# Kernel tuning notes

Measured on AMD Instinct MI355X. Metric: run time of the kernel, lower is better.

## Reference

```python
import jax, jax.numpy as jnp
import numpy as np

DIGITS = 4
SAMPLES = 2048
BATCH = 512
ALPHA = 0.1


def setup_inputs() -> dict:
    key = jax.random.key(0)
    k1, k2, k3 = jax.random.split(key, 3)
    n1_logits = jax.random.normal(k1, (BATCH, DIGITS, 10), dtype=jnp.float32)
    # sample counters start at ones and stay positive; keep them in (1, 2)
    counters = jax.random.uniform(k2, (DIGITS, 10), dtype=jnp.float32) + 1.0
    s = jax.random.randint(k3, (BATCH,), 0, 10 ** DIGITS, dtype=jnp.int32)
    return {"n1_logits": n1_logits, "counters": counters, "s": s}


def reference(n1_logits, counters, s):
    B, D, _ = n1_logits.shape
    S = SAMPLES
    key = jax.random.key(42)
    digit_idx = jnp.arange(10, dtype=jnp.int32)
    constraint = jnp.zeros((B, S), dtype=jnp.int32)
    samples_list = []
    for i in range(D):
        if i == 0:
            maxim = (s // 10 ** (D - 1)).astype(jnp.int32)
            minim = jnp.maximum(0, maxim - 9)
        else:
            maxim = ((s // 10 ** (D - 1 - i)) % 10).astype(jnp.int32)
            minim = jnp.zeros_like(maxim)
        # [B, S, 10]: per-digit logits repeated over samples, counter penalty
        probs = n1_logits[:, i, None, :] - ALPHA * jnp.log(counters[i])[None, None, :]
        probs = jnp.broadcast_to(probs, (B, S, 10))
        # restrict to [minim, maxim] per batch row (equiv of per-row tf.concat with -inf pads)
        valid = (digit_idx[None, :] >= minim[:, None]) & (digit_idx[None, :] <= maxim[:, None])  # [B,10]
        probs_cut = jnp.where(valid[:, None, :], probs, -jnp.inf)
        logits = jnp.where(constraint[..., None] == 1, probs, probs_cut)
        key, sub = jax.random.split(key)
        samp = jax.random.categorical(sub, logits).astype(jnp.int32)  # [B,S]
        constraint = jnp.maximum(jnp.where(samp == maxim[:, None], 0, 1), constraint)
        samples_list.append(samp)
    n1_samples = jnp.stack(samples_list, axis=-1)  # [B,S,D]
    multiplier = (10 ** jnp.arange(D - 1, -1, -1)).astype(jnp.int32)  # [D]
    n1_summed = jnp.sum(n1_samples * multiplier, axis=-1)  # [B,S]
    n2 = s[:, None] - n1_summed  # [B,S], guaranteed in [0, 10^D)
    # sample_weights: per-row multiplicity of each sampled value (unique_with_counts+gather)
    V = 10 ** D
    row = jnp.arange(B, dtype=jnp.int32)[:, None]
    hist = jnp.zeros((B, V), jnp.float32).at[row, n1_summed].add(1.0)
    weights = jnp.take_along_axis(hist, n1_summed, axis=1)  # [B,S]
    # decimalise n2 via cumulative-quotient + sorted shift trick (faithful to tf code)
    mult2 = jnp.concatenate(
        [jnp.full((D - 1,), 10, dtype=jnp.int32), jnp.zeros((1,), dtype=jnp.int32)]
    )  # [10,...,10,0]
    n2d = n2[..., None] // multiplier  # [B,S,D] cumulative quotients
    n2d = n2d - jnp.sort(n2d * mult2, axis=-1)
    return n1_samples[..., None], n2d[..., None], weights
```

## Files before the change

kernel.cpp:

```cpp
#include <hip/hip_runtime.h>
#include <stdint.h>
#include <stddef.h>


namespace {

constexpr int B = 512, S = 2048, D = 4, NC = 10;
constexpr int BS = B * S;
constexpr size_t OUT1_OFF = (size_t)BS * D;
constexpr size_t OUT2_OFF = (size_t)BS * D * 2;

constexpr uint32_t crotl(uint32_t x, int d) { return (x << d) | (x >> (32 - d)); }
struct CU2 { uint32_t a, b; };
constexpr CU2 ctf(uint32_t k0, uint32_t k1, uint32_t c0, uint32_t c1) {
  uint32_t ks2 = k0 ^ k1 ^ 0x1BD11BDAu;
  uint32_t x0 = c0 + k0, x1 = c1 + k1;
  const int rots[8] = {13, 15, 26, 6, 17, 29, 16, 24};
  const uint32_t ks[3] = {k0, k1, ks2};
  for (int blk = 0; blk < 5; ++blk) {
    for (int j = 0; j < 4; ++j) {
      int r = rots[(blk & 1) * 4 + j];
      x0 += x1; x1 = crotl(x1, r); x1 ^= x0;
    }
    x0 += ks[(blk + 1) % 3];
    x1 += ks[(blk + 2) % 3] + (uint32_t)(blk + 1);
  }
  return CU2{x0, x1};
}

struct Keys { uint32_t kx[D]; uint32_t ky[D]; };
constexpr Keys make_keys() {
  Keys K{};
  uint32_t a = 0u, b = 42u;
  for (int i = 0; i < D; ++i) {
    CU2 sub = ctf(a, b, 0u, 1u);
    CU2 nk  = ctf(a, b, 0u, 0u);
    K.kx[i] = sub.a; K.ky[i] = sub.b;
    a = nk.a; b = nk.b;
  }
  return K;
}
constexpr Keys KEYS = make_keys();

struct U2 { uint32_t a, b; };
__device__ __forceinline__ uint32_t rotl32(uint32_t x, int d) {
  return (x << d) | (x >> (32 - d));
}
__device__ __forceinline__ U2 tf(uint32_t k0, uint32_t k1, uint32_t c0, uint32_t c1) {
  uint32_t ks2 = k0 ^ k1 ^ 0x1BD11BDAu;
  uint32_t x0 = c0 + k0, x1 = c1 + k1;
#define TF_RND(r) { x0 += x1; x1 = rotl32(x1, (r)); x1 ^= x0; }
  TF_RND(13) TF_RND(15) TF_RND(26) TF_RND(6)   x0 += k1;  x1 += ks2 + 1u;
  TF_RND(17) TF_RND(29) TF_RND(16) TF_RND(24)  x0 += ks2; x1 += k0 + 2u;
  TF_RND(13) TF_RND(15) TF_RND(26) TF_RND(6)   x0 += k0;  x1 += k1 + 3u;
  TF_RND(17) TF_RND(29) TF_RND(16) TF_RND(24)  x0 += k1;  x1 += ks2 + 4u;
  TF_RND(13) TF_RND(15) TF_RND(26) TF_RND(6)   x0 += ks2; x1 += k0 + 5u;
#undef TF_RND
  return U2{x0, x1};
}

__device__ __forceinline__ float xla_logf(float a) {
  uint32_t bits = __float_as_uint(a);
  float e = (float)((int)(bits >> 23) - 126);
  float m = __uint_as_float((bits & 0x007fffffu) | 0x3f000000u);
  bool mlt = m < 0.707106781186547524f;
  float tmp = mlt ? m : 0.0f;
  float x = __fsub_rn(m, 1.0f);
  e = __fsub_rn(e, mlt ? 1.0f : 0.0f);
  x = __fadd_rn(x, tmp);
  float x2 = __fmul_rn(x, x);
  float x3 = __fmul_rn(x2, x);
  float y  = __fmaf_rn(7.0376836292e-2f,  x, -1.1514610310e-1f);
  float y1 = __fmaf_rn(-1.2420140846e-1f, x,  1.4249322787e-1f);
  float y2 = __fmaf_rn(2.0000714765e-1f,  x, -2.4999993993e-1f);
  y  = __fmaf_rn(y,  x,  1.1676998740e-1f);
  y1 = __fmaf_rn(y1, x, -1.6668057665e-1f);
  y2 = __fmaf_rn(y2, x,  3.3333331174e-1f);
  y  = __fmaf_rn(y, x3, y1);
  y  = __fmaf_rn(y, x3, y2);
  y  = __fmul_rn(y, x3);
  y1 = __fmul_rn(e, -2.12194440e-4f);
  tmp = __fmul_rn(x2, 0.5f);
  y = __fadd_rn(y, y1);
  x = __fsub_rn(x, tmp);
  y2 = __fmul_rn(e, 0.693359375f);
  x = __fadd_rn(x, y);
  x = __fadd_rn(x, y2);
  return x;
}

__device__ __forceinline__ float gumbel_from_bits(uint32_t bits) {
  float f = __fsub_rn(__uint_as_float((bits >> 9) | 0x3f800000u), 1.0f);
  float u = __fadd_rn(f, 1.17549435e-38f);
  float l1 = xla_logf(u);
  float l2 = xla_logf(-l1);
  return -l2;
}

__global__ __launch_bounds__(1024) void fused_kernel(
    const float* __restrict__ logits,
    const float* __restrict__ counters,
    const int*   __restrict__ s_in,
    float* __restrict__ out)
{
  __shared__ int hist[10000];
  __shared__ float s_p[D * NC];
  const int t = threadIdx.x;
  const int b = blockIdx.x;

  for (int i = t; i < 10000; i += 1024) hist[i] = 0;
  if (t < D * NC) {
    s_p[t] = __fsub_rn(logits[b * D * NC + t],
                       __fmul_rn(0.1f, xla_logf(counters[t])));
  }
  __syncthreads();

  const int sval = s_in[b];
  const int mx[D] = {sval / 1000, (sval / 100) % 10, (sval / 10) % 10, sval % 10};

  int vals[2];
#pragma unroll
  for (int k = 0; k < 2; ++k) {
    const int sidx = t + k * 1024;
    const uint32_t n0 = (uint32_t)(b * S + sidx) * (uint32_t)NC;
    int con = 0;
    int dg[D];
#pragma unroll
    for (int i = 0; i < D; ++i) {
      const uint32_t kx = KEYS.kx[i], ky = KEYS.ky[i];
      const int mxi = mx[i];
      float best = -__builtin_inff();
      int bi = 0;
#pragma unroll
      for (int c = 0; c < NC; ++c) {
        U2 r = tf(kx, ky, 0u, n0 + (uint32_t)c);
        float g = gumbel_from_bits(r.a ^ r.b);
        float v = __fadd_rn(g, s_p[i * NC + c]);
        bool allowed = (con != 0) || (c <= mxi);
        if (allowed && v > best) { best = v; bi = c; }
      }
      dg[i] = bi;
      con |= (bi != mxi);
    }

    const int n1v = dg[0] * 1000 + dg[1] * 100 + dg[2] * 10 + dg[3];
    vals[k] = n1v;
    atomicAdd(&hist[n1v], 1);

    const int n2 = sval - n1v;
    const int q0 = n2 / 1000, q1 = (n2 / 100) % 10, q2 = (n2 / 10) % 10, q3 = n2 % 10;

    const size_t o = (size_t)(b * S + sidx) * D;
    *reinterpret_cast<float4*>(out + o) =
        make_float4((float)dg[0], (float)dg[1], (float)dg[2], (float)dg[3]);
    *reinterpret_cast<float4*>(out + OUT1_OFF + o) =
        make_float4((float)q0, (float)q1, (float)q2, (float)q3);
  }

  __syncthreads();
#pragma unroll
  for (int k = 0; k < 2; ++k) {
    const int sidx = t + k * 1024;
    out[OUT2_OFF + (size_t)b * S + sidx] = (float)hist[vals[k]];
  }
}

}

extern "C" void kernel_launch(void* const* d_in, const int* in_sizes, int n_in,
                              void* d_out, int out_size, void* d_ws, size_t ws_size,
                              hipStream_t stream) {
  const float* logits   = (const float*)d_in[0];
  const float* counters = (const float*)d_in[1];
  const int*   s_in     = (const int*)d_in[2];
  float* out = (float*)d_out;

  fused_kernel<<<B, 1024, 0, stream>>>(logits, counters, s_in, out);
}
```

Baseline: 185.3 us.

## Split sampling and histogram into two kernels with compile-time Threefry keys

The fused kernel becomes two. A sampling kernel runs one thread per sample across 4096 blocks of 256 threads. A separate per-row kernel then builds the shared-memory histogram and writes the weights, reading n1 values from workspace or reconstructing them from the output. The Threefry keys become template constants so the key schedule folds at compile time, and the per-digit logits are hoisted into scalar registers with readfirstlane. The goal is better occupancy and less dependence on a 40KB shared histogram per 1024-thread block, at the cost of an extra launch and a global round trip of the n1 values.

Result: faster. 180.3 us (-2.7%).

```diff
diff --git a/kernel.cpp b/kernel.cpp
--- a/kernel.cpp
+++ b/kernel.cpp
@@ -42,21 +42,21 @@
 }
 constexpr Keys KEYS = make_keys();
 
-struct U2 { uint32_t a, b; };
 __device__ __forceinline__ uint32_t rotl32(uint32_t x, int d) {
   return (x << d) | (x >> (32 - d));
 }
-__device__ __forceinline__ U2 tf(uint32_t k0, uint32_t k1, uint32_t c0, uint32_t c1) {
-  uint32_t ks2 = k0 ^ k1 ^ 0x1BD11BDAu;
-  uint32_t x0 = c0 + k0, x1 = c1 + k1;
+template <uint32_t K0, uint32_t K1>
+__device__ __forceinline__ uint32_t tf_xor(uint32_t c1) {
+  constexpr uint32_t KS2 = K0 ^ K1 ^ 0x1BD11BDAu;
+  uint32_t x0 = K0, x1 = c1 + K1;
 #define TF_RND(r) { x0 += x1; x1 = rotl32(x1, (r)); x1 ^= x0; }
-  TF_RND(13) TF_RND(15) TF_RND(26) TF_RND(6)   x0 += k1;  x1 += ks2 + 1u;
-  TF_RND(17) TF_RND(29) TF_RND(16) TF_RND(24)  x0 += ks2; x1 += k0 + 2u;
-  TF_RND(13) TF_RND(15) TF_RND(26) TF_RND(6)   x0 += k0;  x1 += k1 + 3u;
-  TF_RND(17) TF_RND(29) TF_RND(16) TF_RND(24)  x0 += k1;  x1 += ks2 + 4u;
-  TF_RND(13) TF_RND(15) TF_RND(26) TF_RND(6)   x0 += ks2; x1 += k0 + 5u;
+  TF_RND(13) TF_RND(15) TF_RND(26) TF_RND(6)   x0 += K1;  x1 += KS2 + 1u;
+  TF_RND(17) TF_RND(29) TF_RND(16) TF_RND(24)  x0 += KS2; x1 += K0 + 2u;
+  TF_RND(13) TF_RND(15) TF_RND(26) TF_RND(6)   x0 += K0;  x1 += K1 + 3u;
+  TF_RND(17) TF_RND(29) TF_RND(16) TF_RND(24)  x0 += K1;  x1 += KS2 + 4u;
+  TF_RND(13) TF_RND(15) TF_RND(26) TF_RND(6)   x0 += KS2; x1 += K0 + 5u;
 #undef TF_RND
-  return U2{x0, x1};
+  return x0 ^ x1;
 }
 
 __device__ __forceinline__ float xla_logf(float a) {
@@ -97,70 +97,102 @@
   return -l2;
 }
 
-__global__ __launch_bounds__(1024) void fused_kernel(
+__device__ __forceinline__ float sgpr_f(float x) {
+  return __uint_as_float(__builtin_amdgcn_readfirstlane(__float_as_uint(x)));
+}
+
+template <int I>
+__device__ __forceinline__ void do_digit(const float* s_p, uint32_t n0,
+                                         const int* mx, int& con, int* dg) {
+  uint32_t rb[NC];
+#pragma unroll
+  for (int c = 0; c < NC; ++c)
+    rb[c] = tf_xor<KEYS.kx[I], KEYS.ky[I]>(n0 + (uint32_t)c);
+  float sp[NC];
+#pragma unroll
+  for (int c = 0; c < NC; ++c) sp[c] = sgpr_f(s_p[I * NC + c]);
+  const int mxi = mx[I];
+  float best = -__builtin_inff();
+  int bi = 0;
+#pragma unroll
+  for (int c = 0; c < NC; ++c) {
+    float g = gumbel_from_bits(rb[c]);
+    float v = __fadd_rn(g, sp[c]);
+    bool allowed = (con != 0) || (c <= mxi);
+    if (allowed && v > best) { best = v; bi = c; }
+  }
+  dg[I] = bi;
+  con |= (bi != mxi);
+}
+
+__global__ __launch_bounds__(256) void sample_kernel(
     const float* __restrict__ logits,
     const float* __restrict__ counters,
     const int*   __restrict__ s_in,
-    float* __restrict__ out)
+    float* __restrict__ out,
+    int*   __restrict__ n1buf,
+    int    write_ws)
 {
-  __shared__ int hist[10000];
   __shared__ float s_p[D * NC];
   const int t = threadIdx.x;
-  const int b = blockIdx.x;
-
-  for (int i = t; i < 10000; i += 1024) hist[i] = 0;
+  const int blk = blockIdx.x;
+  const int b = blk >> 3;
   if (t < D * NC) {
     s_p[t] = __fsub_rn(logits[b * D * NC + t],
                        __fmul_rn(0.1f, xla_logf(counters[t])));
   }
   __syncthreads();
 
+  const int tid = blk * 256 + t;
   const int sval = s_in[b];
   const int mx[D] = {sval / 1000, (sval / 100) % 10, (sval / 10) % 10, sval % 10};
 
-  int vals[2];
-#pragma unroll
-  for (int k = 0; k < 2; ++k) {
-    const int sidx = t + k * 1024;
-    const uint32_t n0 = (uint32_t)(b * S + sidx) * (uint32_t)NC;
-    int con = 0;
-    int dg[D];
-#pragma unroll
-    for (int i = 0; i < D; ++i) {
-      const uint32_t kx = KEYS.kx[i], ky = KEYS.ky[i];
-      const int mxi = mx[i];
-      float best = -__builtin_inff();
-      int bi = 0;
-#pragma unroll
-      for (int c = 0; c < NC; ++c) {
-        U2 r = tf(kx, ky, 0u, n0 + (uint32_t)c);
-        float g = gumbel_from_bits(r.a ^ r.b);
-        float v = __fadd_rn(g, s_p[i * NC + c]);
-        bool allowed = (con != 0) || (c <= mxi);
-        if (allowed && v > best) { best = v; bi = c; }
-      }
-      dg[i] = bi;
-      con |= (bi != mxi);
+  const uint32_t n0 = (uint32_t)tid * (uint32_t)NC;
+  int con = 0;
+  int dg[D];
+  do_digit<0>(s_p, n0, mx, con, dg);
+  do_digit<1>(s_p, n0, mx, con, dg);
+  do_digit<2>(s_p, n0, mx, con, dg);
+  do_digit<3>(s_p, n0, mx, con, dg);
+
+  const int n1v = dg[0] * 1000 + dg[1] * 100 + dg[2] * 10 + dg[3];
+  const int n2 = sval - n1v;
+  const int q0 = n2 / 1000, q1 = (n2 / 100) % 10, q2 = (n2 / 10) % 10, q3 = n2 % 10;
+
+  const size_t o = (size_t)tid * D;
+  *reinterpret_cast<float4*>(out + o) =
+      make_float4((float)dg[0], (float)dg[1], (float)dg[2], (float)dg[3]);
+  *reinterpret_cast<float4*>(out + OUT1_OFF + o) =
+      make_float4((float)q0, (float)q1, (float)q2, (float)q3);
+  if (write_ws) n1buf[tid] = n1v;
+}
+
+template <bool FROM_WS>
+__global__ __launch_bounds__(256) void weights_kernel(
+    const int* __restrict__ n1buf, float* __restrict__ out) {
+  __shared__ int hist[10000];
+  const int t = threadIdx.x;
+  const int b = blockIdx.x;
+  for (int i = t; i < 10000; i += 256) hist[i] = 0;
+  __syncthreads();
+  int vals[8];
+#pragma unroll
+  for (int k = 0; k < 8; ++k) {
+    const int sidx = t + k * 256;
+    int v;
+    if (FROM_WS) {
+      v = n1buf[b * S + sidx];
+    } else {
+      const float* p = out + ((size_t)(b * S + sidx)) * D;
+      v = 1000 * (int)p[0] + 100 * (int)p[1] + 10 * (int)p[2] + (int)p[3];
     }
-
-    const int n1v = dg[0] * 1000 + dg[1] * 100 + dg[2] * 10 + dg[3];
-    vals[k] = n1v;
-    atomicAdd(&hist[n1v], 1);
-
-    const int n2 = sval - n1v;
-    const int q0 = n2 / 1000, q1 = (n2 / 100) % 10, q2 = (n2 / 10) % 10, q3 = n2 % 10;
-
-    const size_t o = (size_t)(b * S + sidx) * D;
-    *reinterpret_cast<float4*>(out + o) =
-        make_float4((float)dg[0], (float)dg[1], (float)dg[2], (float)dg[3]);
-    *reinterpret_cast<float4*>(out + OUT1_OFF + o) =
-        make_float4((float)q0, (float)q1, (float)q2, (float)q3);
-  }
-
+    vals[k] = v;
+    atomicAdd(&hist[v], 1);
+  }
   __syncthreads();
 #pragma unroll
-  for (int k = 0; k < 2; ++k) {
-    const int sidx = t + k * 1024;
+  for (int k = 0; k < 8; ++k) {
+    const int sidx = t + k * 256;
     out[OUT2_OFF + (size_t)b * S + sidx] = (float)hist[vals[k]];
   }
 }
@@ -174,6 +206,11 @@
   const float* counters = (const float*)d_in[1];
   const int*   s_in     = (const int*)d_in[2];
   float* out = (float*)d_out;
-
-  fused_kernel<<<B, 1024, 0, stream>>>(logits, counters, s_in, out);
-}
+  int*   n1buf = (int*)d_ws;
+  const int use_ws = (d_ws != nullptr && ws_size >= (size_t)BS * sizeof(int)) ? 1 : 0;
+
+  sample_kernel<<<BS / 256, 256, 0, stream>>>(logits, counters, s_in, out,
+                                              n1buf, use_ws);
+  if (use_ws) weights_kernel<true><<<B, 256, 0, stream>>>(n1buf, out);
+  else        weights_kernel<false><<<B, 256, 0, stream>>>(nullptr, out);
+}
```
